# Performance work log

Hardware: AMD Instinct MI355X
Metric: run time of the kernel (lower is better)

Reference implementation:

```python
import math
import jax, jax.numpy as jnp
import numpy as np

HEAD_DIM = 128
N_HEADS = 64    # n_local_heads
N_KV = 8        # n_local_kv_heads
N_REP = 8       # GQA group size


def setup_inputs() -> dict:
    key = jax.random.key(0)
    ks = jax.random.split(key, 6)
    bsz, seqlen, d = 32, 1, 8192
    start_pos = 4095
    T = start_pos + seqlen  # 4096 total KV length
    x = jax.random.normal(ks[0], (bsz, seqlen, d), jnp.float32)
    wqkv_w = jax.random.normal(ks[1], (8192, 10240), jnp.float32) * 0.02  # used as x @ W
    wo_w = jax.random.normal(ks[2], (8192, 8192), jnp.float32) * 0.02    # torch Linear weight (out,in)
    theta = jax.random.uniform(ks[3], (seqlen, HEAD_DIM // 2), jnp.float32) * (2.0 * np.pi)
    freqs_cos = jnp.cos(theta)
    freqs_sin = jnp.sin(theta)
    cache_k = jax.random.normal(ks[4], (bsz, T, N_KV, HEAD_DIM), jnp.float32)
    cache_v = jax.random.normal(ks[5], (bsz, T, N_KV, HEAD_DIM), jnp.float32)
    mask = jnp.zeros((1, 1, 1, T), jnp.float32)
    return {"x": x, "cache_k": cache_k, "cache_v": cache_v, "wqkv_w": wqkv_w,
            "wo_w": wo_w, "freqs_cos": freqs_cos, "freqs_sin": freqs_sin,
            "mask": mask, "start_pos": start_pos}


def _rope(t, cos, sin):
    # t: [b, s, h, d]; cos/sin: [s, d//2]. Complex mult on interleaved (re, im) pairs.
    tr = t.reshape(*t.shape[:-1], -1, 2)
    c = cos[None, :, None, :]
    s = sin[None, :, None, :]
    re = tr[..., 0] * c - tr[..., 1] * s
    im = tr[..., 0] * s + tr[..., 1] * c
    return jnp.stack([re, im], axis=-1).reshape(t.shape)


def reference(x, cache_k, cache_v, wqkv_w, wo_w, freqs_cos, freqs_sin, mask, start_pos):
    bsz, seqlen, _ = x.shape
    blk_q = N_REP * HEAD_DIM  # 1024
    blk = blk_q + HEAD_DIM + HEAD_DIM  # 1280: interleaved q|k|v block
    # fused qkv projection, then split interleaved blocks
    xqkv = jnp.einsum('bsd,dn->bsn', x, wqkv_w).reshape(bsz, seqlen, -1, blk)
    xq = xqkv[..., :blk_q].reshape(bsz, seqlen, N_HEADS, HEAD_DIM)
    xk = xqkv[..., blk_q:blk_q + HEAD_DIM].reshape(bsz, seqlen, N_KV, HEAD_DIM)
    xv = xqkv[..., blk_q + HEAD_DIM:].reshape(bsz, seqlen, N_KV, HEAD_DIM)
    # rotary embedding on q and k
    xq = _rope(xq, freqs_cos, freqs_sin)
    xk = _rope(xk, freqs_cos, freqs_sin)
    # KV-cache write
    cache_k = jax.lax.dynamic_update_slice(cache_k, xk, (0, start_pos, 0, 0))
    cache_v = jax.lax.dynamic_update_slice(cache_v, xv, (0, start_pos, 0, 0))
    T = start_pos + seqlen
    keys = cache_k[:, :T]     # [b, T, kv, d]
    values = cache_v[:, :T]
    # GQA: group q-heads by kv-head instead of materializing repeat_kv (same math)
    q = xq.transpose(0, 2, 1, 3).reshape(bsz, N_KV, N_REP, seqlen, HEAD_DIM)
    scores = jnp.einsum('bkrsd,btkd->bkrst', q, keys) / math.sqrt(HEAD_DIM)
    scores = scores + mask  # mask [1,1,1,T] broadcasts over (r, s, t)
    probs = jax.nn.softmax(scores, axis=-1)
    out = jnp.einsum('bkrst,btkd->bkrsd', probs, values)
    out = out.reshape(bsz, N_HEADS, seqlen, HEAD_DIM).transpose(0, 2, 1, 3).reshape(bsz, seqlen, -1)
    return out @ wo_w.T
```

## Files before the change

### kernel.cpp

```cpp
#include <hip/hip_runtime.h>
#include <hip/hip_bf16.h>
#include <math.h>

typedef float  f32x4 __attribute__((ext_vector_type(4)));
typedef short  s16x8 __attribute__((ext_vector_type(8)));
typedef unsigned int u32;

#define B_   32
#define D_   8192
#define NQ   10240
#define T_   4096
#define NKV  8
#define HD   128
#define BLKW 1280
#define KSPLIT 16
#define KC   512

__device__ inline short f2bf(float f) {
  union { float f; unsigned u; } v; v.f = f;
  unsigned r = (v.u + 0x7FFFu + ((v.u >> 16) & 1u)) >> 16;
  return (short)r;
}

__device__ inline s16x8 pack8(float4 a, float4 b) {
  s16x8 r;
  r[0]=f2bf(a.x); r[1]=f2bf(a.y); r[2]=f2bf(a.z); r[3]=f2bf(a.w);
  r[4]=f2bf(b.x); r[5]=f2bf(b.y); r[6]=f2bf(b.z); r[7]=f2bf(b.w);
  return r;
}

__global__ __launch_bounds__(256) void k_qkv(const float* __restrict__ x,
                                             const float* __restrict__ W,
                                             float* __restrict__ p1) {
  int tid  = threadIdx.x;
  int lane = tid & 63, wv = tid >> 6;
  int l15  = lane & 15, lg = lane >> 4;
  int n0   = blockIdx.x * 128 + wv * 32;
  int k0   = blockIdx.y * KC;

  f32x4 acc00 = (f32x4)0.f, acc01 = (f32x4)0.f;
  f32x4 acc10 = (f32x4)0.f, acc11 = (f32x4)0.f;

  const float* xr0 = x + (size_t)l15 * D_ + k0 + lg * 8;
  const float* xr1 = x + (size_t)(16 + l15) * D_ + k0 + lg * 8;
  const float* wc0 = W + (size_t)k0 * NQ + n0 + l15;

  #pragma unroll 2
  for (int ks = 0; ks < KC; ks += 32) {
    float4 a0a = *(const float4*)(xr0 + ks);
    float4 a0b = *(const float4*)(xr0 + ks + 4);
    float4 a1a = *(const float4*)(xr1 + ks);
    float4 a1b = *(const float4*)(xr1 + ks + 4);
    const float* wk = wc0 + (size_t)(ks + lg * 8) * NQ;
    float w0[8], w1[8];
    #pragma unroll
    for (int j = 0; j < 8; ++j) {
      w0[j] = wk[(size_t)j * NQ];
      w1[j] = wk[(size_t)j * NQ + 16];
    }
    s16x8 af0 = pack8(a0a, a0b);
    s16x8 af1 = pack8(a1a, a1b);
    s16x8 bf0, bf1;
    #pragma unroll
    for (int j = 0; j < 8; ++j) { bf0[j] = f2bf(w0[j]); bf1[j] = f2bf(w1[j]); }
    acc00 = __builtin_amdgcn_mfma_f32_16x16x32_bf16(af0, bf0, acc00, 0, 0, 0);
    acc01 = __builtin_amdgcn_mfma_f32_16x16x32_bf16(af0, bf1, acc01, 0, 0, 0);
    acc10 = __builtin_amdgcn_mfma_f32_16x16x32_bf16(af1, bf0, acc10, 0, 0, 0);
    acc11 = __builtin_amdgcn_mfma_f32_16x16x32_bf16(af1, bf1, acc11, 0, 0, 0);
  }

  size_t base = (size_t)(blockIdx.y * 32) * NQ;
  #pragma unroll
  for (int r = 0; r < 4; ++r) {
    p1[base + (size_t)(lg * 4 + r) * NQ + n0 + l15]           = acc00[r];
    p1[base + (size_t)(lg * 4 + r) * NQ + n0 + 16 + l15]      = acc01[r];
    p1[base + (size_t)(16 + lg * 4 + r) * NQ + n0 + l15]      = acc10[r];
    p1[base + (size_t)(16 + lg * 4 + r) * NQ + n0 + 16 + l15] = acc11[r];
  }
}

__global__ void k_reduce_rope(const float* __restrict__ p1,
                              const float* __restrict__ fcos, const float* __restrict__ fsin,
                              float* __restrict__ qs, float* __restrict__ knew,
                              float* __restrict__ vnew) {
  int b = blockIdx.y;
  int j = (blockIdx.x * 256 + threadIdx.x) * 2;
  float v0 = 0.f, v1 = 0.f;
  #pragma unroll
  for (int c = 0; c < KSPLIT; ++c) {
    const float2 p = *(const float2*)(p1 + (size_t)(c * 32 + b) * NQ + j);
    v0 += p.x; v1 += p.y;
  }
  int g = j / BLKW;
  int r = j - g * BLKW;
  if (r < 1024) {
    int h = r >> 7, d = r & 127, dp = d >> 1;
    float c = fcos[dp], s = fsin[dp];
    const float sc = 0.08838834764831845f;
    float* q = qs + ((size_t)(b * NKV + g) * 8 + h) * HD + d;
    q[0] = (v0 * c - v1 * s) * sc;
    q[1] = (v0 * s + v1 * c) * sc;
  } else if (r < 1152) {
    int d = r - 1024, dp = d >> 1;
    float c = fcos[dp], s = fsin[dp];
    float* kp = knew + (size_t)(b * NKV + g) * HD + d;
    kp[0] = v0 * c - v1 * s;
    kp[1] = v0 * s + v1 * c;
  } else {
    int d = r - 1152;
    float* vp = vnew + (size_t)(b * NKV + g) * HD + d;
    vp[0] = v0; vp[1] = v1;
  }
}

__global__ __launch_bounds__(256, 4) void k_attn(const float* __restrict__ cK,
                                                 const float* __restrict__ cV,
                                                 const float* __restrict__ qs,
                                                 const float* __restrict__ knew,
                                                 const float* __restrict__ vnew,
                                                 float* __restrict__ pml,
                                                 float* __restrict__ pacc) {
  __shared__ __align__(16) short Plds[4][2][16][32];
  int bid  = blockIdx.x;
  int pair = bid >> 2, tc = bid & 3;
  int b = pair >> 3, kv = pair & 7;
  int tid = threadIdx.x;
  int w = tid >> 6, lane = tid & 63;
  int l15 = lane & 15, lg = lane >> 4;

  for (int idx = lane; idx < 512; idx += 64) {
    int buf = idx >> 8, rem = idx & 255;
    Plds[w][buf][8 + (rem >> 5)][rem & 31] = 0;
  }

  s16x8 aq[4];
  const float* qrow = qs + ((size_t)(b * NKV + kv) * 8 + l15) * HD;
  #pragma unroll
  for (int dt = 0; dt < 4; ++dt) {
    if (l15 < 8) {
      float4 fa = *(const float4*)(qrow + dt * 32 + lg * 8);
      float4 fb = *(const float4*)(qrow + dt * 32 + lg * 8 + 4);
      aq[dt] = pack8(fa, fb);
    } else {
      s16x8 z = {0,0,0,0,0,0,0,0};
      aq[dt] = z;
    }
  }

  float m[4], lsum[4];
  #pragma unroll
  for (int r = 0; r < 4; ++r) { m[r] = -INFINITY; lsum[r] = 0.f; }
  f32x4 acc[8];
  #pragma unroll
  for (int dt = 0; dt < 8; ++dt) acc[dt] = (f32x4)0.f;

  const size_t bkv_off = (size_t)b * T_ * NKV * HD + (size_t)kv * HD;
  const float* knp = knew + (size_t)(b * NKV + kv) * HD;
  const float* vnp = vnew + (size_t)(b * NKV + kv) * HD;

  for (int tile = 0; tile < 8; ++tile) {
    int t0 = tc * 1024 + (w * 8 + tile) * 32;
    int pb = tile & 1;

    f32x4 s0 = (f32x4)0.f, s1 = (f32x4)0.f;
    {
      int trow = t0 + l15;
      const float* krow = (trow == 4095) ? knp : (cK + bkv_off + (size_t)trow * (NKV * HD));
      #pragma unroll
      for (int dt = 0; dt < 4; ++dt) {
        float4 fa = *(const float4*)(krow + dt * 32 + lg * 8);
        float4 fb = *(const float4*)(krow + dt * 32 + lg * 8 + 4);
        s16x8 bk = pack8(fa, fb);
        s0 = __builtin_amdgcn_mfma_f32_16x16x32_bf16(aq[dt], bk, s0, 0, 0, 0);
      }
    }
    {
      int trow = t0 + 16 + l15;
      const float* krow = (trow == 4095) ? knp : (cK + bkv_off + (size_t)trow * (NKV * HD));
      #pragma unroll
      for (int dt = 0; dt < 4; ++dt) {
        float4 fa = *(const float4*)(krow + dt * 32 + lg * 8);
        float4 fb = *(const float4*)(krow + dt * 32 + lg * 8 + 4);
        s16x8 bk = pack8(fa, fb);
        s1 = __builtin_amdgcn_mfma_f32_16x16x32_bf16(aq[dt], bk, s1, 0, 0, 0);
      }
    }

    float p0[4], p1v[4], scale[4];
    #pragma unroll
    for (int r = 0; r < 4; ++r) {
      float tm = fmaxf(s0[r], s1[r]);
      #pragma unroll
      for (int off = 1; off < 16; off <<= 1) tm = fmaxf(tm, __shfl_xor(tm, off));
      float mn = fmaxf(m[r], tm);
      scale[r] = __expf(m[r] - mn);
      p0[r]  = __expf(s0[r] - mn);
      p1v[r] = __expf(s1[r] - mn);
      float rsum = p0[r] + p1v[r];
      #pragma unroll
      for (int off = 1; off < 16; off <<= 1) rsum += __shfl_xor(rsum, off);
      lsum[r] = lsum[r] * scale[r] + rsum;
      m[r] = mn;
    }
    #pragma unroll
    for (int dt = 0; dt < 8; ++dt) {
      #pragma unroll
      for (int r = 0; r < 4; ++r) acc[dt][r] *= scale[r];
    }

    if (lg < 2) {
      #pragma unroll
      for (int r = 0; r < 4; ++r) {
        int h = lg * 4 + r;
        Plds[w][pb][h][l15]      = f2bf(p0[r]);
        Plds[w][pb][h][16 + l15] = f2bf(p1v[r]);
      }
    }
    s16x8 ap = *(const s16x8*)&Plds[w][pb][l15][lg * 8];

    const float* vrow[8];
    #pragma unroll
    for (int jj = 0; jj < 8; ++jj) {
      int tr = t0 + lg * 8 + jj;
      vrow[jj] = (tr == 4095) ? vnp : (cV + bkv_off + (size_t)tr * (NKV * HD));
    }
    #pragma unroll
    for (int dt = 0; dt < 8; ++dt) {
      s16x8 bv;
      #pragma unroll
      for (int jj = 0; jj < 8; ++jj) bv[jj] = f2bf(vrow[jj][dt * 16 + l15]);
      acc[dt] = __builtin_amdgcn_mfma_f32_16x16x32_bf16(ap, bv, acc[dt], 0, 0, 0);
    }
  }

  int widx = bid * 4 + w;
  if (lg < 2) {
    #pragma unroll
    for (int r = 0; r < 4; ++r) {
      int h = lg * 4 + r;
      if (l15 == 0) {
        pml[widx * 16 + h]     = m[r];
        pml[widx * 16 + 8 + h] = lsum[r];
      }
      #pragma unroll
      for (int dt = 0; dt < 8; ++dt)
        pacc[(size_t)widx * 1024 + h * 128 + dt * 16 + l15] = acc[dt][r];
    }
  }
}

__global__ void k_attn_combine(const float* __restrict__ pml,
                               const float* __restrict__ pacc,
                               float* __restrict__ o) {
  int pair = blockIdx.x;
  int tid = threadIdx.x;
  #pragma unroll
  for (int cc = 0; cc < 4; ++cc) {
    int cell = cc * 256 + tid;
    int h = cell >> 7;
    float mstar = -INFINITY;
    #pragma unroll
    for (int w2 = 0; w2 < 16; ++w2)
      mstar = fmaxf(mstar, pml[(pair * 16 + w2) * 16 + h]);
    float L = 0.f, val = 0.f;
    #pragma unroll
    for (int w2 = 0; w2 < 16; ++w2) {
      float mw = pml[(pair * 16 + w2) * 16 + h];
      float lw = pml[(pair * 16 + w2) * 16 + 8 + h];
      float f = __expf(mw - mstar);
      L += lw * f;
      val += f * pacc[(size_t)(pair * 16 + w2) * 1024 + cell];
    }
    o[(size_t)pair * 1024 + cell] = val / L;
  }
}

__global__ __launch_bounds__(256) void k_oproj(const float* __restrict__ o,
                                               const float* __restrict__ wo,
                                               float* __restrict__ p2) {
  int tid = threadIdx.x;
  int w = tid >> 6, lane = tid & 63, l15 = lane & 15, lg = lane >> 4;
  int i0 = blockIdx.x * 64 + w * 16;
  int jc = blockIdx.y * 1024;
  f32x4 acc0 = (f32x4)0.f, acc1 = (f32x4)0.f;
  const float* orow0 = o + (size_t)l15 * D_;
  const float* orow1 = o + (size_t)(16 + l15) * D_;
  const float* wrow  = wo + (size_t)(i0 + l15) * D_;
  for (int j = jc; j < jc + 1024; j += 32) {
    int off = j + lg * 8;
    float4 a0 = *(const float4*)(orow0 + off), a0b = *(const float4*)(orow0 + off + 4);
    float4 a1 = *(const float4*)(orow1 + off), a1b = *(const float4*)(orow1 + off + 4);
    float4 b0 = *(const float4*)(wrow + off),  b0b = *(const float4*)(wrow + off + 4);
    s16x8 fa0 = pack8(a0, a0b);
    s16x8 fa1 = pack8(a1, a1b);
    s16x8 fb  = pack8(b0, b0b);
    acc0 = __builtin_amdgcn_mfma_f32_16x16x32_bf16(fa0, fb, acc0, 0, 0, 0);
    acc1 = __builtin_amdgcn_mfma_f32_16x16x32_bf16(fa1, fb, acc1, 0, 0, 0);
  }
  size_t base = (size_t)blockIdx.y * (B_ * D_);
  #pragma unroll
  for (int r = 0; r < 4; ++r) {
    p2[base + (size_t)(lg * 4 + r) * D_ + i0 + l15]      = acc0[r];
    p2[base + (size_t)(16 + lg * 4 + r) * D_ + i0 + l15] = acc1[r];
  }
}

__global__ void k_final(const float* __restrict__ p2, float* __restrict__ out) {
  int g = blockIdx.x * 256 + threadIdx.x;
  float s = 0.f;
  #pragma unroll
  for (int c = 0; c < 8; ++c) s += p2[(size_t)c * (B_ * D_) + g];
  out[g] = s;
}

extern "C" void kernel_launch(void* const* d_in, const int* in_sizes, int n_in,
                              void* d_out, int out_size, void* d_ws, size_t ws_size,
                              hipStream_t stream) {
  const float* x    = (const float*)d_in[0];
  const float* cK   = (const float*)d_in[1];
  const float* cV   = (const float*)d_in[2];
  const float* wqkv = (const float*)d_in[3];
  const float* wo   = (const float*)d_in[4];
  const float* fcos = (const float*)d_in[5];
  const float* fsin = (const float*)d_in[6];

  float* W = (float*)d_ws;
  float* qs     = W + 262144;
  float* knew   = W + 524288;
  float* vnew   = W + 557056;
  float* o      = W + 589824;
  float* shared = W + 851968;
  float* p1   = shared;
  float* pml  = shared;
  float* pacc = shared + 65536;
  float* p2   = shared;
  float* outF = (float*)d_out;

  k_qkv<<<dim3(80, KSPLIT), 256, 0, stream>>>(x, wqkv, p1);
  k_reduce_rope<<<dim3(20, 32), 256, 0, stream>>>(p1, fcos, fsin, qs, knew, vnew);
  k_attn<<<1024, 256, 0, stream>>>(cK, cV, qs, knew, vnew, pml, pacc);
  k_attn_combine<<<256, 256, 0, stream>>>(pml, pacc, o);
  k_oproj<<<dim3(128, 8), 256, 0, stream>>>(o, wo, p2);
  k_final<<<1024, 256, 0, stream>>>(p2, outF);
}
```

Before: 405.5 us.

## Widen QKV GEMM per-wave column tile and double the K-split

The QKV projection kernel now gives each wave 128 output columns (eight 16-wide MFMA groups) instead of 32, and halves the K chunk so the split-K factor doubles to 32. The aim is to keep more independent weight loads in flight per wave and raise memory-level parallelism on the large fp32 weight stream, with launch bounds hinting at 4 blocks per CU. In exchange the split-K partial buffer doubles, adding write and read traffic in the reduce kernel, and the larger accumulator array raises register pressure. The wider partial buffer could also exceed the workspace region set aside for it.

```diff
diff --git a/kernel.cpp b/kernel.cpp
--- a/kernel.cpp
+++ b/kernel.cpp
@@ -13,8 +13,8 @@
 #define NKV  8
 #define HD   128
 #define BLKW 1280
-#define KSPLIT 16
-#define KC   512
+#define KSPLIT 32
+#define KC   256
 
 __device__ inline short f2bf(float f) {
   union { float f; unsigned u; } v; v.f = f;
@@ -29,53 +29,53 @@
   return r;
 }
 
-__global__ __launch_bounds__(256) void k_qkv(const float* __restrict__ x,
-                                             const float* __restrict__ W,
-                                             float* __restrict__ p1) {
+__global__ __launch_bounds__(256, 4) void k_qkv(const float* __restrict__ x,
+                                                const float* __restrict__ W,
+                                                float* __restrict__ p1) {
   int tid  = threadIdx.x;
   int lane = tid & 63, wv = tid >> 6;
   int l15  = lane & 15, lg = lane >> 4;
-  int n0   = blockIdx.x * 128 + wv * 32;
+  int nw   = blockIdx.x * 512 + wv * 128;
   int k0   = blockIdx.y * KC;
 
-  f32x4 acc00 = (f32x4)0.f, acc01 = (f32x4)0.f;
-  f32x4 acc10 = (f32x4)0.f, acc11 = (f32x4)0.f;
+  f32x4 acc0[8], acc1[8];
+  #pragma unroll
+  for (int g = 0; g < 8; ++g) { acc0[g] = (f32x4)0.f; acc1[g] = (f32x4)0.f; }
 
   const float* xr0 = x + (size_t)l15 * D_ + k0 + lg * 8;
   const float* xr1 = x + (size_t)(16 + l15) * D_ + k0 + lg * 8;
-  const float* wc0 = W + (size_t)k0 * NQ + n0 + l15;
-
-  #pragma unroll 2
+  const float* wc0 = W + (size_t)k0 * NQ + nw + l15;
+
   for (int ks = 0; ks < KC; ks += 32) {
     float4 a0a = *(const float4*)(xr0 + ks);
     float4 a0b = *(const float4*)(xr0 + ks + 4);
     float4 a1a = *(const float4*)(xr1 + ks);
     float4 a1b = *(const float4*)(xr1 + ks + 4);
-    const float* wk = wc0 + (size_t)(ks + lg * 8) * NQ;
-    float w0[8], w1[8];
-    #pragma unroll
-    for (int j = 0; j < 8; ++j) {
-      w0[j] = wk[(size_t)j * NQ];
-      w1[j] = wk[(size_t)j * NQ + 16];
-    }
     s16x8 af0 = pack8(a0a, a0b);
     s16x8 af1 = pack8(a1a, a1b);
-    s16x8 bf0, bf1;
-    #pragma unroll
-    for (int j = 0; j < 8; ++j) { bf0[j] = f2bf(w0[j]); bf1[j] = f2bf(w1[j]); }
-    acc00 = __builtin_amdgcn_mfma_f32_16x16x32_bf16(af0, bf0, acc00, 0, 0, 0);
-    acc01 = __builtin_amdgcn_mfma_f32_16x16x32_bf16(af0, bf1, acc01, 0, 0, 0);
-    acc10 = __builtin_amdgcn_mfma_f32_16x16x32_bf16(af1, bf0, acc10, 0, 0, 0);
-    acc11 = __builtin_amdgcn_mfma_f32_16x16x32_bf16(af1, bf1, acc11, 0, 0, 0);
+
+    const float* wk = wc0 + (size_t)(ks + lg * 8) * NQ;
+    #pragma unroll
+    for (int g = 0; g < 8; ++g) {
+      float wvv[8];
+      #pragma unroll
+      for (int j = 0; j < 8; ++j) wvv[j] = wk[(size_t)j * NQ + g * 16];
+      s16x8 bf;
+      #pragma unroll
+      for (int j = 0; j < 8; ++j) bf[j] = f2bf(wvv[j]);
+      acc0[g] = __builtin_amdgcn_mfma_f32_16x16x32_bf16(af0, bf, acc0[g], 0, 0, 0);
+      acc1[g] = __builtin_amdgcn_mfma_f32_16x16x32_bf16(af1, bf, acc1[g], 0, 0, 0);
+    }
   }
 
   size_t base = (size_t)(blockIdx.y * 32) * NQ;
   #pragma unroll
-  for (int r = 0; r < 4; ++r) {
-    p1[base + (size_t)(lg * 4 + r) * NQ + n0 + l15]           = acc00[r];
-    p1[base + (size_t)(lg * 4 + r) * NQ + n0 + 16 + l15]      = acc01[r];
-    p1[base + (size_t)(16 + lg * 4 + r) * NQ + n0 + l15]      = acc10[r];
-    p1[base + (size_t)(16 + lg * 4 + r) * NQ + n0 + 16 + l15] = acc11[r];
+  for (int g = 0; g < 8; ++g) {
+    #pragma unroll
+    for (int r = 0; r < 4; ++r) {
+      p1[base + (size_t)(lg * 4 + r) * NQ + nw + g * 16 + l15]      = acc0[g][r];
+      p1[base + (size_t)(16 + lg * 4 + r) * NQ + nw + g * 16 + l15] = acc1[g][r];
+    }
   }
 }
 
@@ -336,7 +336,7 @@
   float* p2   = shared;
   float* outF = (float*)d_out;
 
-  k_qkv<<<dim3(80, KSPLIT), 256, 0, stream>>>(x, wqkv, p1);
+  k_qkv<<<dim3(20, KSPLIT), 256, 0, stream>>>(x, wqkv, p1);
   k_reduce_rope<<<dim3(20, 32), 256, 0, stream>>>(p1, fcos, fsin, qs, knew, vnew);
   k_attn<<<1024, 256, 0, stream>>>(cK, cV, qs, knew, vnew, pml, pacc);
   k_attn_combine<<<256, 256, 0, stream>>>(pml, pacc, o);
```

After: 415.7 us. 1.03x slower.
